# Kernel optimization log

Hardware: AMD Instinct MI355X
Metric: run time of the kernel (lower is better)

Reference implementation:

```python
import jax, jax.numpy as jnp
import numpy as np

N, E, P, IN, H = 1024, 65536, 1024, 128, 64
LN_EPS = 1e-5


def _layernorm(x, g, b):
    mu = x.mean(-1, keepdims=True)
    var = ((x - mu) ** 2).mean(-1, keepdims=True)
    return (x - mu) * jax.lax.rsqrt(var + LN_EPS) * g + b


def _gcn(x, ei, W, b, n):
    # PyG GCNConv: out = D^{-1/2} (A + I) D^{-1/2} X W + b
    row, col = ei[0], ei[1]
    xw = x @ W
    deg = jnp.zeros((n,), xw.dtype).at[col].add(1.0) + 1.0  # self-loop adds 1
    dinv = jax.lax.rsqrt(deg)
    coef = (dinv[row] * dinv[col])[:, None]
    out = jnp.zeros_like(xw).at[col].add(xw[row] * coef)
    out = out + xw * (dinv * dinv)[:, None]  # self-loop message
    return out + b


def setup_inputs() -> dict:
    key = jax.random.key(0)
    ks = jax.random.split(key, 20)
    f32 = jnp.float32
    inp = {
        "x": jax.random.normal(ks[0], (N, IN), f32),
        "ei": jax.random.randint(ks[1], (2, E), 0, N, dtype=jnp.int32),
        "pos": jax.random.randint(ks[2], (2, P), 0, N, dtype=jnp.int32),
        # GCNConv(input, hidden) and GCNConv(hidden, hidden)
        "W_g1": jax.random.normal(ks[3], (IN, H), f32) * (IN ** -0.5),
        "b_g1": jnp.zeros((H,), f32),
        "W_g2": jax.random.normal(ks[4], (H, H), f32) * (H ** -0.5),
        "b_g2": jnp.zeros((H,), f32),
        # mlp1: Linear + LayerNorm (+Dropout eval=id) + ReLU
        "W_m1": jax.random.normal(ks[5], (H, H), f32) * (H ** -0.5),
        "b_m1": jnp.zeros((H,), f32),
        "g_m1": jnp.ones((H,), f32),
        "be_m1": jnp.zeros((H,), f32),
        # mlp2
        "W_m2": jax.random.normal(ks[6], (H, H), f32) * (H ** -0.5),
        "b_m2": jnp.zeros((H,), f32),
        "g_m2": jnp.ones((H,), f32),
        "be_m2": jnp.zeros((H,), f32),
        # mlp3: Linear(2H,H) + ReLU + Linear(H,1)
        "W_a": jax.random.normal(ks[7], (2 * H, H), f32) * ((2 * H) ** -0.5),
        "b_a": jnp.zeros((H,), f32),
        "W_b": jax.random.normal(ks[8], (H, 1), f32) * (H ** -0.5),
        "b_b": jnp.zeros((1,), f32),
    }
    return inp


def reference(x, ei, pos, W_g1, b_g1, W_g2, b_g2, W_m1, b_m1, g_m1, be_m1,
              W_m2, b_m2, g_m2, be_m2, W_a, b_a, W_b, b_b):
    n = x.shape[0]
    # forward_routine
    h = _gcn(x, ei, W_g1, b_g1, n)
    h = _gcn(h, ei, W_g2, b_g2, n)
    xx = h[pos[0]] * h[pos[1]]          # [P, H] pairwise node products at queries
    xe = h[ei[0]] * h[ei[1]]            # [E, H] pairwise node products at edges
    x1 = jax.nn.relu(_layernorm(xe @ W_m1 + b_m1, g_m1, be_m1))  # mlp1
    x2 = jax.nn.relu(_layernorm(xe @ W_m2 + b_m2, g_m2, be_m2))  # mlp2
    # dense_bmm / sparse_bmm followed by combine() keeps only entries at pos
    # pairs, so compute res[pos0, pos1, :] = sum_k D1[pos0, k, :] * D2[k, pos1, :]
    D1 = jnp.zeros((n, n, H), x2.dtype).at[ei[0], ei[1]].set(x2)  # mlp2 output: left operand
    D2 = jnp.zeros((n, n, H), x1.dtype).at[ei[0], ei[1]].set(x1)  # mlp1 output: right operand
    r1 = D1[pos[0]]                                   # [P, N, H]
    c2 = jnp.swapaxes(jnp.take(D2, pos[1], axis=1), 0, 1)  # [P, N, H]
    pos_val = jnp.einsum('pnh,pnh->ph', r1, c2)       # [P, H]
    feat = jnp.concatenate([pos_val, xx], axis=1)     # combine -> [P, 2H]
    hid = jax.nn.relu(feat @ W_a + b_a)               # mlp3 (dropout = identity at eval)
    return (hid @ W_b + b_b).squeeze(-1)              # [P]
```

## Files before the change

### kernel.cpp

```cpp
#include <hip/hip_runtime.h>

#define Nn 1024
#define Ee 65536
#define Pq 1024
#define CAP 160

typedef unsigned long long ull;

__global__ __launch_bounds__(256) void k_front(const float* __restrict__ x,
                                               const float* __restrict__ Wg1,
                                               float* __restrict__ xw1,
                                               const int* __restrict__ ei,
                                               int* __restrict__ degI,
                                               int* __restrict__ adj,
                                               ull* __restrict__ Mbit,
                                               ull* __restrict__ MTbit) {
    __shared__ float sW[8192];
    int tid = threadIdx.x;
    int gid = blockIdx.x * 256 + tid;
    for (int i = tid; i < 8192; i += 256) sW[i] = Wg1[i];
    __syncthreads();
    {
        int lane = gid & 63;
        int r = __builtin_amdgcn_readfirstlane(gid >> 6);
        const float* xr = x + r * 128;
        float acc = 0.f;
        #pragma unroll 8
        for (int j = 0; j < 128; ++j) acc = fmaf(xr[j], sW[j * 64 + lane], acc);
        xw1[gid] = acc;
    }
    {
        int r = ei[gid], c = ei[Ee + gid];
        int slot = atomicAdd(&degI[c], 1);
        if (slot < CAP) adj[c * CAP + slot] = r;
        atomicOr(&Mbit[r * 16 + (c >> 6)], 1ull << (c & 63));
        atomicOr(&MTbit[c * 16 + (r >> 6)], 1ull << (r & 63));
    }
}

__device__ __forceinline__ float gather_quarter(const int* __restrict__ adj,
                                                const float* __restrict__ xwsrc,
                                                const float* s_dinv, int c, int w,
                                                int n, int lane) {
    const int* al = adj + c * CAP;
    float acc = 0.f;
    int j = w, end = n;
    for (; j + 12 < end; j += 16) {
        int r0 = al[j], r1 = al[j + 4], r2 = al[j + 8], r3 = al[j + 12];
        float a0 = xwsrc[r0 * 64 + lane] * s_dinv[r0];
        float a1 = xwsrc[r1 * 64 + lane] * s_dinv[r1];
        float a2 = xwsrc[r2 * 64 + lane] * s_dinv[r2];
        float a3 = xwsrc[r3 * 64 + lane] * s_dinv[r3];
        acc += (a0 + a1) + (a2 + a3);
    }
    for (; j < end; j += 4) {
        int r = al[j];
        acc += xwsrc[r * 64 + lane] * s_dinv[r];
    }
    return acc;
}

__global__ __launch_bounds__(256) void k_gather1(const int* __restrict__ adj,
                                                 const int* __restrict__ degI,
                                                 const float* __restrict__ xw1,
                                                 const float* __restrict__ Wg2,
                                                 const float* __restrict__ bg1,
                                                 float* __restrict__ xw2) {
    __shared__ float sW[4096];
    __shared__ float s_dinv[Nn];
    __shared__ float red[4][64];
    int tid = threadIdx.x;
    int lane = tid & 63;
    int w = tid >> 6;
    int c = blockIdx.x;
    for (int i = tid; i < 4096; i += 256) sW[i] = Wg2[i];
    for (int i = tid; i < Nn; i += 256) s_dinv[i] = rsqrtf((float)degI[i] + 1.f);
    __syncthreads();
    int n = __builtin_amdgcn_readfirstlane(degI[c]);
    if (n > CAP) n = CAP;
    float acc = gather_quarter(adj, xw1, s_dinv, c, w, n, lane);
    red[w][lane] = acc;
    __syncthreads();
    if (w == 0) {
        float a = (red[0][lane] + red[1][lane]) + (red[2][lane] + red[3][lane]);
        float dc = s_dinv[c];
        float h1c = dc * a + dc * dc * xw1[c * 64 + lane] + bg1[lane];
        float t = 0.f;
        #pragma unroll 8
        for (int j = 0; j < 64; ++j) t = fmaf(__shfl(h1c, j), sW[j * 64 + lane], t);
        xw2[c * 64 + lane] = t;
    }
}

__global__ __launch_bounds__(256) void k_gather2(const int* __restrict__ adj,
                                                 const int* __restrict__ degI,
                                                 const float* __restrict__ xw2,
                                                 const float* __restrict__ bg2,
                                                 float* __restrict__ h2) {
    __shared__ float s_dinv[Nn];
    __shared__ float red[4][64];
    int tid = threadIdx.x;
    int lane = tid & 63;
    int w = tid >> 6;
    int c = blockIdx.x;
    for (int i = tid; i < Nn; i += 256) s_dinv[i] = rsqrtf((float)degI[i] + 1.f);
    __syncthreads();
    int n = __builtin_amdgcn_readfirstlane(degI[c]);
    if (n > CAP) n = CAP;
    float acc = gather_quarter(adj, xw2, s_dinv, c, w, n, lane);
    red[w][lane] = acc;
    __syncthreads();
    if (w == 0) {
        float a = (red[0][lane] + red[1][lane]) + (red[2][lane] + red[3][lane]);
        float dc = s_dinv[c];
        h2[c * 64 + lane] = dc * a + dc * dc * xw2[c * 64 + lane] + bg2[lane];
    }
}

__global__ __launch_bounds__(128) void k_posfinal(
    const int* __restrict__ pos,
    const ull* __restrict__ Mbit, const ull* __restrict__ MTbit,
    const float* __restrict__ h2,
    const float* __restrict__ W1, const float* __restrict__ b1,
    const float* __restrict__ g1, const float* __restrict__ be1,
    const float* __restrict__ W2, const float* __restrict__ b2,
    const float* __restrict__ g2, const float* __restrict__ be2,
    const float* __restrict__ Wa, const float* __restrict__ ba,
    const float* __restrict__ Wb, const float* __restrict__ bb,
    float* __restrict__ out) {
    __shared__ float W1s[4096], W2s[4096];
    int tid = threadIdx.x;
    for (int i = tid; i < 4096; i += 128) { W1s[i] = W1[i]; W2s[i] = W2[i]; }
    __syncthreads();
    int lane = tid & 63;
    int w = tid >> 6;
    int p = blockIdx.x * 2 + w;
    int a = __builtin_amdgcn_readfirstlane(pos[p]);
    int b = __builtin_amdgcn_readfirstlane(pos[Pq + p]);
    float ha = h2[a * 64 + lane], hb = h2[b * 64 + lane];
    float lb1 = b1[lane], lg1 = g1[lane], lbe1 = be1[lane];
    float lb2 = b2[lane], lg2 = g2[lane], lbe2 = be2[lane];
    float acc = 0.f;
    for (int wd = 0; wd < 16; ++wd) {
        ull bits = Mbit[a * 16 + wd] & MTbit[b * 16 + wd];
        while (bits) {
            int k = (wd << 6) + __ffsll(bits) - 1;
            bits &= bits - 1;
            float hk = h2[k * 64 + lane];
            float xeA = ha * hk;
            float xeB = hk * hb;
            float a2 = lb2, a1 = lb1;
            #pragma unroll 8
            for (int j = 0; j < 64; ++j) {
                float vA = __shfl(xeA, j);
                float vB = __shfl(xeB, j);
                a2 = fmaf(vA, W2s[j * 64 + lane], a2);
                a1 = fmaf(vB, W1s[j * 64 + lane], a1);
            }
            float s2 = a2, q2 = a2 * a2, s1 = a1, q1 = a1 * a1;
            for (int off = 32; off; off >>= 1) {
                s2 += __shfl_xor(s2, off); q2 += __shfl_xor(q2, off);
                s1 += __shfl_xor(s1, off); q1 += __shfl_xor(q1, off);
            }
            float mu2 = s2 * (1.f / 64.f), mu1 = s1 * (1.f / 64.f);
            float v2 = q2 * (1.f / 64.f) - mu2 * mu2;
            float v1 = q1 * (1.f / 64.f) - mu1 * mu1;
            float r2v = rsqrtf(v2 + 1e-5f), r1v = rsqrtf(v1 + 1e-5f);
            float x2v = fmaxf(0.f, (a2 - mu2) * r2v * lg2 + lbe2);
            float x1v = fmaxf(0.f, (a1 - mu1) * r1v * lg1 + lbe1);
            acc += x2v * x1v;
        }
    }
    float xx = ha * hb;
    float t = ba[lane];
    #pragma unroll 8
    for (int j = 0; j < 64; ++j) {
        t = fmaf(__shfl(acc, j), Wa[j * 64 + lane], t);
        t = fmaf(__shfl(xx, j), Wa[(64 + j) * 64 + lane], t);
    }
    t = fmaxf(t, 0.f);
    float v = t * Wb[lane];
    for (int off = 32; off; off >>= 1) v += __shfl_xor(v, off);
    if (lane == 0) out[p] = v + bb[0];
}

extern "C" void kernel_launch(void* const* d_in, const int* in_sizes, int n_in,
                              void* d_out, int out_size, void* d_ws, size_t ws_size,
                              hipStream_t stream) {
    const float* x    = (const float*)d_in[0];
    const int*   ei   = (const int*)d_in[1];
    const int*   pos  = (const int*)d_in[2];
    const float* Wg1  = (const float*)d_in[3];
    const float* bg1  = (const float*)d_in[4];
    const float* Wg2  = (const float*)d_in[5];
    const float* bg2  = (const float*)d_in[6];
    const float* Wm1  = (const float*)d_in[7];
    const float* bm1  = (const float*)d_in[8];
    const float* gm1  = (const float*)d_in[9];
    const float* bem1 = (const float*)d_in[10];
    const float* Wm2  = (const float*)d_in[11];
    const float* bm2  = (const float*)d_in[12];
    const float* gm2  = (const float*)d_in[13];
    const float* bem2 = (const float*)d_in[14];
    const float* Wa   = (const float*)d_in[15];
    const float* ba   = (const float*)d_in[16];
    const float* Wb   = (const float*)d_in[17];
    const float* bb   = (const float*)d_in[18];
    float* out = (float*)d_out;

    char* w = (char*)d_ws;
    char* zbase = w;
    int* degI = (int*)w;  w += 1024 * 4;
    ull* Mbit = (ull*)w;  w += 1024 * 16 * 8;
    ull* MTbit = (ull*)w; w += 1024 * 16 * 8;
    size_t zbytes = (size_t)(w - zbase);
    int*   adj = (int*)w;   w += (size_t)Nn * CAP * 4;
    float* xw1 = (float*)w; w += 65536 * 4;
    float* xw2 = (float*)w; w += 65536 * 4;
    float* h2  = (float*)w; w += 65536 * 4;

    hipMemsetAsync(zbase, 0, zbytes, stream);

    k_front<<<256, 256, 0, stream>>>(x, Wg1, xw1, ei, degI, adj, Mbit, MTbit);
    k_gather1<<<Nn, 256, 0, stream>>>(adj, degI, xw1, Wg2, bg1, xw2);
    k_gather2<<<Nn, 256, 0, stream>>>(adj, degI, xw2, bg2, h2);
    k_posfinal<<<Pq / 2, 128, 0, stream>>>(pos, Mbit, MTbit, h2,
                                           Wm1, bm1, gm1, bem1,
                                           Wm2, bm2, gm2, bem2,
                                           Wa, ba, Wb, bb, out);
}
```

Before: 69.28 us.

## Split pos-pair bitmask scan across two waves, vectorize smem loads, deepen gather unroll

The pos-pair kernel now uses 256 threads per block, with two wavefronts per query pair that each scan alternating bitmask words, then combine partial sums through shared memory before the final MLP. Weight and degree staging loads switch to float4/int4 vector accesses, and the GCN gather loop is unrolled to eight neighbours per iteration. The aim is more parallelism and latency hiding in the intersection loop, which is load-imbalanced, plus fewer load instructions. The costs are an extra block barrier and higher register pressure in the gather.

```diff
diff --git a/kernel.cpp b/kernel.cpp
--- a/kernel.cpp
+++ b/kernel.cpp
@@ -18,7 +18,8 @@
     __shared__ float sW[8192];
     int tid = threadIdx.x;
     int gid = blockIdx.x * 256 + tid;
-    for (int i = tid; i < 8192; i += 256) sW[i] = Wg1[i];
+    for (int i = tid; i < 2048; i += 256)
+        ((float4*)sW)[i] = ((const float4*)Wg1)[i];
     __syncthreads();
     {
         int lane = gid & 63;
@@ -45,13 +46,18 @@
     const int* al = adj + c * CAP;
     float acc = 0.f;
     int j = w, end = n;
-    for (; j + 12 < end; j += 16) {
-        int r0 = al[j], r1 = al[j + 4], r2 = al[j + 8], r3 = al[j + 12];
+    for (; j + 28 < end; j += 32) {
+        int r0 = al[j],      r1 = al[j + 4],  r2 = al[j + 8],  r3 = al[j + 12];
+        int r4 = al[j + 16], r5 = al[j + 20], r6 = al[j + 24], r7 = al[j + 28];
         float a0 = xwsrc[r0 * 64 + lane] * s_dinv[r0];
         float a1 = xwsrc[r1 * 64 + lane] * s_dinv[r1];
         float a2 = xwsrc[r2 * 64 + lane] * s_dinv[r2];
         float a3 = xwsrc[r3 * 64 + lane] * s_dinv[r3];
-        acc += (a0 + a1) + (a2 + a3);
+        float a4 = xwsrc[r4 * 64 + lane] * s_dinv[r4];
+        float a5 = xwsrc[r5 * 64 + lane] * s_dinv[r5];
+        float a6 = xwsrc[r6 * 64 + lane] * s_dinv[r6];
+        float a7 = xwsrc[r7 * 64 + lane] * s_dinv[r7];
+        acc += ((a0 + a1) + (a2 + a3)) + ((a4 + a5) + (a6 + a7));
     }
     for (; j < end; j += 4) {
         int r = al[j];
@@ -73,8 +79,15 @@
     int lane = tid & 63;
     int w = tid >> 6;
     int c = blockIdx.x;
-    for (int i = tid; i < 4096; i += 256) sW[i] = Wg2[i];
-    for (int i = tid; i < Nn; i += 256) s_dinv[i] = rsqrtf((float)degI[i] + 1.f);
+    for (int i = tid; i < 1024; i += 256)
+        ((float4*)sW)[i] = ((const float4*)Wg2)[i];
+    {
+        int4 d4 = ((const int4*)degI)[tid];
+        s_dinv[4 * tid]     = rsqrtf((float)d4.x + 1.f);
+        s_dinv[4 * tid + 1] = rsqrtf((float)d4.y + 1.f);
+        s_dinv[4 * tid + 2] = rsqrtf((float)d4.z + 1.f);
+        s_dinv[4 * tid + 3] = rsqrtf((float)d4.w + 1.f);
+    }
     __syncthreads();
     int n = __builtin_amdgcn_readfirstlane(degI[c]);
     if (n > CAP) n = CAP;
@@ -103,7 +116,13 @@
     int lane = tid & 63;
     int w = tid >> 6;
     int c = blockIdx.x;
-    for (int i = tid; i < Nn; i += 256) s_dinv[i] = rsqrtf((float)degI[i] + 1.f);
+    {
+        int4 d4 = ((const int4*)degI)[tid];
+        s_dinv[4 * tid]     = rsqrtf((float)d4.x + 1.f);
+        s_dinv[4 * tid + 1] = rsqrtf((float)d4.y + 1.f);
+        s_dinv[4 * tid + 2] = rsqrtf((float)d4.z + 1.f);
+        s_dinv[4 * tid + 3] = rsqrtf((float)d4.w + 1.f);
+    }
     __syncthreads();
     int n = __builtin_amdgcn_readfirstlane(degI[c]);
     if (n > CAP) n = CAP;
@@ -117,7 +136,7 @@
     }
 }
 
-__global__ __launch_bounds__(128) void k_posfinal(
+__global__ __launch_bounds__(256) void k_posfinal(
     const int* __restrict__ pos,
     const ull* __restrict__ Mbit, const ull* __restrict__ MTbit,
     const float* __restrict__ h2,
@@ -129,19 +148,25 @@
     const float* __restrict__ Wb, const float* __restrict__ bb,
     float* __restrict__ out) {
     __shared__ float W1s[4096], W2s[4096];
-    int tid = threadIdx.x;
-    for (int i = tid; i < 4096; i += 128) { W1s[i] = W1[i]; W2s[i] = W2[i]; }
+    __shared__ float s_red[2][64];
+    int tid = threadIdx.x;
+    for (int i = tid; i < 1024; i += 256) {
+        ((float4*)W1s)[i] = ((const float4*)W1)[i];
+        ((float4*)W2s)[i] = ((const float4*)W2)[i];
+    }
     __syncthreads();
     int lane = tid & 63;
-    int w = tid >> 6;
-    int p = blockIdx.x * 2 + w;
+    int wv = tid >> 6;
+    int q = wv >> 1;
+    int half = wv & 1;
+    int p = blockIdx.x * 2 + q;
     int a = __builtin_amdgcn_readfirstlane(pos[p]);
     int b = __builtin_amdgcn_readfirstlane(pos[Pq + p]);
     float ha = h2[a * 64 + lane], hb = h2[b * 64 + lane];
     float lb1 = b1[lane], lg1 = g1[lane], lbe1 = be1[lane];
     float lb2 = b2[lane], lg2 = g2[lane], lbe2 = be2[lane];
     float acc = 0.f;
-    for (int wd = 0; wd < 16; ++wd) {
+    for (int wd = half; wd < 16; wd += 2) {
         ull bits = Mbit[a * 16 + wd] & MTbit[b * 16 + wd];
         while (bits) {
             int k = (wd << 6) + __ffsll(bits) - 1;
@@ -171,17 +196,22 @@
             acc += x2v * x1v;
         }
     }
-    float xx = ha * hb;
-    float t = ba[lane];
-    #pragma unroll 8
-    for (int j = 0; j < 64; ++j) {
-        t = fmaf(__shfl(acc, j), Wa[j * 64 + lane], t);
-        t = fmaf(__shfl(xx, j), Wa[(64 + j) * 64 + lane], t);
-    }
-    t = fmaxf(t, 0.f);
-    float v = t * Wb[lane];
-    for (int off = 32; off; off >>= 1) v += __shfl_xor(v, off);
-    if (lane == 0) out[p] = v + bb[0];
+    if (half) s_red[q][lane] = acc;
+    __syncthreads();
+    if (!half) {
+        acc += s_red[q][lane];
+        float xx = ha * hb;
+        float t = ba[lane];
+        #pragma unroll 8
+        for (int j = 0; j < 64; ++j) {
+            t = fmaf(__shfl(acc, j), Wa[j * 64 + lane], t);
+            t = fmaf(__shfl(xx, j), Wa[(64 + j) * 64 + lane], t);
+        }
+        t = fmaxf(t, 0.f);
+        float v = t * Wb[lane];
+        for (int off = 32; off; off >>= 1) v += __shfl_xor(v, off);
+        if (lane == 0) out[p] = v + bb[0];
+    }
 }
 
 extern "C" void kernel_launch(void* const* d_in, const int* in_sizes, int n_in,
@@ -224,7 +254,7 @@
     k_front<<<256, 256, 0, stream>>>(x, Wg1, xw1, ei, degI, adj, Mbit, MTbit);
     k_gather1<<<Nn, 256, 0, stream>>>(adj, degI, xw1, Wg2, bg1, xw2);
     k_gather2<<<Nn, 256, 0, stream>>>(adj, degI, xw2, bg2, h2);
-    k_posfinal<<<Pq / 2, 128, 0, stream>>>(pos, Mbit, MTbit, h2,
+    k_posfinal<<<Pq / 2, 256, 0, stream>>>(pos, Mbit, MTbit, h2,
                                            Wm1, bm1, gm1, bem1,
                                            Wm2, bm2, gm2, bem2,
                                            Wa, ba, Wb, bb, out);
```

Result: faster. 64.85 us (-6.4%).
